# Optimization experiments

Measured on AMD Instinct MI355X. Metric: run time of the kernel, lower is better.

Reference implementation:

```python
import jax, jax.numpy as jnp
import numpy as np

DIM = 1024
HEADS = 16
SCALE = DIM ** (-0.5)  # NOTE: module scales by full dim, not head_dim


def setup_inputs() -> dict:
    key = jax.random.key(0)
    k1, k2, k3, k4 = jax.random.split(key, 4)
    x = jax.random.normal(k1, (4, 2048, DIM), dtype=jnp.float32)
    # torch Linear weights: y = x @ W.T
    w_qkv = jax.random.normal(k2, (3 * DIM, DIM), dtype=jnp.float32) * (DIM ** -0.5)
    w_out = jax.random.normal(k3, (DIM, DIM), dtype=jnp.float32) * (DIM ** -0.5)
    b_out = jax.random.normal(k4, (DIM,), dtype=jnp.float32) * 0.01
    return {"x": x, "w_qkv": w_qkv, "w_out": w_out, "b_out": b_out}


def reference(x, w_qkv, w_out, b_out):
    b, n, _ = x.shape
    h = HEADS
    d = DIM // h
    qkv = x @ w_qkv.T                                   # [b, n, 3*dim]
    qkv = qkv.reshape(b, n, 3, h, d)                    # split (qkv h d)
    qkv = jnp.transpose(qkv, (2, 0, 3, 1, 4))           # [3, b, h, n, d]
    q, k, v = qkv[0], qkv[1], qkv[2]
    dots = jnp.einsum('bhid,bhjd->bhij', q, k) * SCALE  # [b, h, n, n]
    attn = jax.nn.softmax(dots, axis=-1)
    out = jnp.einsum('bhij,bhjd->bhid', attn, v)        # [b, h, n, d]
    out = jnp.transpose(out, (0, 2, 1, 3)).reshape(b, n, h * d)
    return out @ w_out.T + b_out
```

## Files before the change

### kernel.cpp

```cpp
#include <hip/hip_runtime.h>

typedef short bf16x8 __attribute__((ext_vector_type(8)));
typedef _Float16 f16x8 __attribute__((ext_vector_type(8)));
typedef __fp16 fp16x2 __attribute__((ext_vector_type(2)));
typedef float f32x4 __attribute__((ext_vector_type(4)));
typedef float f32x16 __attribute__((ext_vector_type(16)));
typedef unsigned u32x2 __attribute__((ext_vector_type(2)));

static __device__ __forceinline__ unsigned short f2bf(float f) {
  union { float f; unsigned u; } v; v.f = f;
  unsigned r = v.u + 0x7fffu + ((v.u >> 16) & 1u);
  return (unsigned short)(r >> 16);
}

static __device__ __forceinline__ unsigned short f2h(float f) {
  union { _Float16 h; unsigned short u; } c; c.h = (_Float16)f; return c.u;
}

static __device__ __forceinline__ unsigned pkh(float lo, float hi) {
  union { fp16x2 h; unsigned u; } c;
  c.h = __builtin_amdgcn_cvt_pkrtz(lo, hi);
  return c.u;
}

static __device__ __forceinline__ void gll16(const unsigned short* g,
                                             unsigned short* l) {
  __builtin_amdgcn_global_load_lds(
      (const __attribute__((address_space(1))) unsigned int*)g,
      (__attribute__((address_space(3))) unsigned int*)l, 16, 0, 0);
}

__global__ void cvt3_kernel(const float* __restrict__ a,
                            const float* __restrict__ b,
                            const float* __restrict__ c,
                            unsigned short* __restrict__ dst) {
  int i = blockIdx.x * blockDim.x + threadIdx.x;
  const float* src; int off;
  if (i < 2097152) { src = a; off = 0; }
  else if (i < 2883584) { src = b; off = 2097152; }
  else { src = c; off = 2883584; }
  float4 f = ((const float4*)src)[i - off];
  ushort4 o;
  o.x = f2bf(f.x); o.y = f2bf(f.y); o.z = f2bf(f.z); o.w = f2bf(f.w);
  ((ushort4*)dst)[i] = o;
}

#define TM 128
#define TN 128
#define BK 64

template <int EPI>
__global__ __launch_bounds__(256, 2)
void gemm_bt(const unsigned short* __restrict__ X,
             const unsigned short* __restrict__ W,
             unsigned short* __restrict__ QKV, float* __restrict__ OUT,
             const float* __restrict__ bias, int M, int N, int K) {
  __shared__ __align__(16) unsigned short As[TM * BK];
  __shared__ __align__(16) unsigned short Bs[TN * BK];

  const int tid = threadIdx.x;
  const int lane = tid & 63;
  const int wave = tid >> 6;
  const int quad = lane >> 4;
  const int l16 = lane & 15;
  const int wm = wave >> 1, wn = wave & 1;
  const int rc = l16 & 7;

  const int m0 = blockIdx.y * TM;
  const int n0 = blockIdx.x * TN;

  const int sr = lane >> 3;
  const int gsc = ((lane & 7) ^ sr) * 8;

  f32x4 zero = {0.f, 0.f, 0.f, 0.f};
  f32x4 acc[4][4];
#pragma unroll
  for (int i = 0; i < 4; i++)
#pragma unroll
    for (int j = 0; j < 4; j++) acc[i][j] = zero;

  for (int k0 = 0; k0 < K; k0 += BK) {
    __syncthreads();
#pragma unroll
    for (int c = 0; c < 4; c++) {
      int row = wave * 32 + c * 8;
      gll16(&X[(size_t)(m0 + row + sr) * K + k0 + gsc], &As[row * BK]);
      gll16(&W[(size_t)(n0 + row + sr) * K + k0 + gsc], &Bs[row * BK]);
    }
    __syncthreads();
#pragma unroll
    for (int kk = 0; kk < 2; kk++) {
      bf16x8 af[4], bfr[4];
      const int csw = ((kk * 4 + quad) ^ rc) * 8;
#pragma unroll
      for (int t = 0; t < 4; t++) {
        af[t]  = *(const bf16x8*)&As[(wm * 64 + t * 16 + l16) * BK + csw];
        bfr[t] = *(const bf16x8*)&Bs[(wn * 64 + t * 16 + l16) * BK + csw];
      }
#pragma unroll
      for (int mt = 0; mt < 4; mt++)
#pragma unroll
        for (int nt = 0; nt < 4; nt++)
          acc[mt][nt] = __builtin_amdgcn_mfma_f32_16x16x32_bf16(
              af[mt], bfr[nt], acc[mt][nt], 0, 0, 0);
    }
  }

#pragma unroll
  for (int mt = 0; mt < 4; mt++) {
#pragma unroll
    for (int nt = 0; nt < 4; nt++) {
      if (EPI == 0) {
        int nbase = n0 + wn * 64 + nt * 16;
        int which = nbase >> 10;
        if (which == 2) {
          int rem = (nbase + l16) & 1023;
          int h = rem >> 6, dd = rem & 63;
          int growb = m0 + wm * 64 + mt * 16 + quad * 4;
          int b = growb >> 11, nn0 = growb & 2047;
          ushort4 o;
          o.x = f2h(acc[mt][nt][0]);
          o.y = f2h(acc[mt][nt][1]);
          o.z = f2h(acc[mt][nt][2]);
          o.w = f2h(acc[mt][nt][3]);
          *(ushort4*)&QKV[16777216u + (((size_t)(b * 16 + h) * 64 + dd) << 11) + nn0] = o;
        } else {
#pragma unroll
          for (int r = 0; r < 4; r++) {
            int grow = m0 + wm * 64 + mt * 16 + quad * 4 + r;
            int gcol = nbase + l16;
            int rem = gcol & 1023;
            int h = rem >> 6, dd = rem & 63;
            float v = acc[mt][nt][r];
            if (which == 0) v *= 0.04508422f;
            int b = grow >> 11, nn = grow & 2047;
            QKV[(size_t)which * 8388608 +
                ((size_t)(b * 16 + h) * 2048 + nn) * 64 + dd] = f2bf(v);
          }
        }
      } else {
#pragma unroll
        for (int r = 0; r < 4; r++) {
          int grow = m0 + wm * 64 + mt * 16 + quad * 4 + r;
          int gcol = n0 + wn * 64 + nt * 16 + l16;
          OUT[(size_t)grow * N + gcol] = acc[mt][nt][r] + bias[gcol];
        }
      }
    }
  }
}

#define SK 72

__global__ __launch_bounds__(512, 4)
void attn_kernel(const unsigned short* __restrict__ Qg,
                 const unsigned short* __restrict__ Kg,
                 const unsigned short* __restrict__ Vg,
                 unsigned short* __restrict__ AO) {
  __shared__ __align__(16) unsigned short K_s[2][64 * SK];
  __shared__ __align__(16) unsigned short V_s[2][64 * SK];

  const int tid = threadIdx.x;
  const int lane = tid & 63;
  const int wave = tid >> 6;
  const int l31 = lane & 31;
  const int hh = lane >> 5;

  const int id = blockIdx.x + 8 * blockIdx.y;
  const int xcd = id & 7;
  const int slot = id >> 3;
  const int bh = xcd * 8 + (slot & 7);
  const int qb = slot >> 3;

  const size_t base = (size_t)bh * 131072;
  const int q0 = qb * 256 + wave * 32;

  bf16x8 bq[4];
#pragma unroll
  for (int ks = 0; ks < 4; ks++)
    bq[ks] = *(const bf16x8*)&Qg[base + (size_t)(q0 + l31) * 64 + ks * 16 + hh * 8];

  f32x16 O[2];
#pragma unroll
  for (int dt = 0; dt < 2; dt++)
#pragma unroll
    for (int r = 0; r < 16; r++) O[dt][r] = 0.f;
  float lrow = 0.f;

  const int sr = lane >> 3, sc = (lane & 7) * 8;
  const unsigned short* Kp = Kg + base + (size_t)(wave * 8 + sr) * 64 + sc;
  const unsigned short* Vp = Vg + base + (size_t)(wave * 8 + sr) * 2048 + sc;
  const int woff = (wave * 8 + sr) * SK + sc;

  uint4 kr, vr;
  kr = *(const uint4*)Kp;
  vr = *(const uint4*)Vp;
  *(uint4*)&K_s[0][woff] = kr;
  *(uint4*)&V_s[0][woff] = vr;
  __syncthreads();

  for (int t = 0; t < 32; t++) {
    const unsigned short* Kc = K_s[t & 1];
    const unsigned short* Vc = V_s[t & 1];
    if (t < 31) {
      kr = *(const uint4*)(Kp + (size_t)(t + 1) * 4096);
      vr = *(const uint4*)(Vp + (size_t)(t + 1) * 64);
    }

    f32x16 S[2];
#pragma unroll
    for (int sub = 0; sub < 2; sub++) {
      f32x16 a;
#pragma unroll
      for (int r = 0; r < 16; r++) a[r] = 0.f;
#pragma unroll
      for (int ks = 0; ks < 4; ks++) {
        bf16x8 kf = *(const bf16x8*)&Kc[(sub * 32 + l31) * SK + ks * 16 + hh * 8];
        a = __builtin_amdgcn_mfma_f32_32x32x16_bf16(kf, bq[ks], a, 0, 0, 0);
      }
      S[sub] = a;
    }

    float rsum = 0.f;
#pragma unroll
    for (int sub = 0; sub < 2; sub++)
#pragma unroll
      for (int r = 0; r < 16; r++) {
        float p = __builtin_amdgcn_exp2f(S[sub][r]);
        S[sub][r] = p;
        rsum += p;
      }
    lrow += rsum;

#pragma unroll
    for (int win = 0; win < 4; win++) {
      const int sub = win >> 1, kk = win & 1;
      const int g0 = kk * 2, g1 = kk * 2 + 1;
      unsigned a00 = pkh(S[sub][4 * g0 + 0], S[sub][4 * g0 + 1]);
      unsigned a01 = pkh(S[sub][4 * g0 + 2], S[sub][4 * g0 + 3]);
      unsigned a10 = pkh(S[sub][4 * g1 + 0], S[sub][4 * g1 + 1]);
      unsigned a11 = pkh(S[sub][4 * g1 + 2], S[sub][4 * g1 + 3]);
      union { unsigned u[4]; f16x8 v; } fr;
#if __has_builtin(__builtin_amdgcn_permlane32_swap)
      u32x2 r0 = __builtin_amdgcn_permlane32_swap(a00, a10, false, false);
      u32x2 r1 = __builtin_amdgcn_permlane32_swap(a01, a11, false, false);
      fr.u[0] = r0.x; fr.u[1] = r1.x; fr.u[2] = r0.y; fr.u[3] = r1.y;
#else
      unsigned b00 = __shfl_xor((int)a00, 32);
      unsigned b01 = __shfl_xor((int)a01, 32);
      unsigned b10 = __shfl_xor((int)a10, 32);
      unsigned b11 = __shfl_xor((int)a11, 32);
      fr.u[0] = hh ? b10 : a00;
      fr.u[1] = hh ? b11 : a01;
      fr.u[2] = hh ? a10 : b00;
      fr.u[3] = hh ? a11 : b01;
#endif
      f16x8 pf = fr.v;
#pragma unroll
      for (int dt = 0; dt < 2; dt++) {
        f16x8 vf = *(const f16x8*)&Vc[(dt * 32 + l31) * SK + win * 16 + hh * 8];
        O[dt] = __builtin_amdgcn_mfma_f32_32x32x16_f16(vf, pf, O[dt], 0, 0, 0);
      }
    }

    if (t < 31) {
      const int nb = (t + 1) & 1;
      *(uint4*)&K_s[nb][woff] = kr;
      *(uint4*)&V_s[nb][woff] = vr;
    }
    __syncthreads();
  }

  const int b4 = bh >> 4, head = bh & 15;
  lrow += __shfl_xor(lrow, 32);
  float inv = 1.0f / lrow;
  int row = b4 * 2048 + q0 + l31;
#pragma unroll
  for (int dt = 0; dt < 2; dt++)
#pragma unroll
    for (int g = 0; g < 4; g++) {
      ushort4 o;
      o.x = f2bf(O[dt][4 * g + 0] * inv);
      o.y = f2bf(O[dt][4 * g + 1] * inv);
      o.z = f2bf(O[dt][4 * g + 2] * inv);
      o.w = f2bf(O[dt][4 * g + 3] * inv);
      *(ushort4*)&AO[(size_t)row * 1024 + head * 64 + dt * 32 + 8 * g + 4 * hh] = o;
    }
}

extern "C" void kernel_launch(void* const* d_in, const int* in_sizes, int n_in,
                              void* d_out, int out_size, void* d_ws,
                              size_t ws_size, hipStream_t stream) {
  const float* x     = (const float*)d_in[0];
  const float* w_qkv = (const float*)d_in[1];
  const float* w_out = (const float*)d_in[2];
  const float* b_out = (const float*)d_in[3];
  float* out = (float*)d_out;

  unsigned short* ws = (unsigned short*)d_ws;
  unsigned short* Xbf  = ws;
  unsigned short* Wqkv = ws + 8388608;
  unsigned short* Wout = ws + 11534336;
  unsigned short* QKV  = ws + 12582912;
  unsigned short* AO   = ws;

  cvt3_kernel<<<12288, 256, 0, stream>>>(x, w_qkv, w_out, Xbf);

  gemm_bt<0><<<dim3(3072 / TN, 8192 / TM), 256, 0, stream>>>(
      Xbf, Wqkv, QKV, nullptr, nullptr, 8192, 3072, 1024);

  attn_kernel<<<dim3(8, 64), 512, 0, stream>>>(
      QKV, QKV + 8388608, QKV + 16777216, AO);

  gemm_bt<1><<<dim3(1024 / TN, 8192 / TM), 256, 0, stream>>>(
      AO, Wout, nullptr, out, b_out, 8192, 1024, 1024);
}
```

Before: 251.2 us.

## Halve attention block size to 4 waves and add MFMA priority hints

The attention kernel now runs 256-thread blocks covering 128 queries each, in a 16x64 grid, and remaps block ids so the XCD grouping still works. Each thread stages two K/V rows per tile to fill the 64-row shared buffers. The MFMA sections are wrapped in s_setprio raises, and the first QK MFMA takes a zero constant instead of an explicitly zeroed accumulator. The intent is more, smaller blocks per CU for better scheduling and less barrier stall per block, at the cost of twice the K/V loads from global memory per query.

```diff
diff --git a/kernel.cpp b/kernel.cpp
--- a/kernel.cpp
+++ b/kernel.cpp
@@ -152,7 +152,7 @@
 
 #define SK 72
 
-__global__ __launch_bounds__(512, 4)
+__global__ __launch_bounds__(256, 4)
 void attn_kernel(const unsigned short* __restrict__ Qg,
                  const unsigned short* __restrict__ Kg,
                  const unsigned short* __restrict__ Vg,
@@ -166,60 +166,66 @@
   const int l31 = lane & 31;
   const int hh = lane >> 5;
 
-  const int id = blockIdx.x + 8 * blockIdx.y;
+  const int id = blockIdx.x + 16 * blockIdx.y;
   const int xcd = id & 7;
   const int slot = id >> 3;
   const int bh = xcd * 8 + (slot & 7);
   const int qb = slot >> 3;
 
   const size_t base = (size_t)bh * 131072;
-  const int q0 = qb * 256 + wave * 32;
+  const int q0 = qb * 128 + wave * 32;
 
   bf16x8 bq[4];
 #pragma unroll
   for (int ks = 0; ks < 4; ks++)
     bq[ks] = *(const bf16x8*)&Qg[base + (size_t)(q0 + l31) * 64 + ks * 16 + hh * 8];
 
+  f32x16 z16;
+#pragma unroll
+  for (int r = 0; r < 16; r++) z16[r] = 0.f;
+
   f32x16 O[2];
 #pragma unroll
-  for (int dt = 0; dt < 2; dt++)
-#pragma unroll
-    for (int r = 0; r < 16; r++) O[dt][r] = 0.f;
+  for (int dt = 0; dt < 2; dt++) O[dt] = z16;
   float lrow = 0.f;
 
   const int sr = lane >> 3, sc = (lane & 7) * 8;
-  const unsigned short* Kp = Kg + base + (size_t)(wave * 8 + sr) * 64 + sc;
-  const unsigned short* Vp = Vg + base + (size_t)(wave * 8 + sr) * 2048 + sc;
-  const int woff = (wave * 8 + sr) * SK + sc;
-
-  uint4 kr, vr;
-  kr = *(const uint4*)Kp;
-  vr = *(const uint4*)Vp;
-  *(uint4*)&K_s[0][woff] = kr;
-  *(uint4*)&V_s[0][woff] = vr;
+  const int r0 = wave * 8 + sr;
+  const unsigned short* Kp = Kg + base + (size_t)r0 * 64 + sc;
+  const unsigned short* Vp = Vg + base + (size_t)r0 * 2048 + sc;
+  const int woff = r0 * SK + sc;
+
+  uint4 kr0, kr1, vr0, vr1;
+  kr0 = *(const uint4*)Kp;           kr1 = *(const uint4*)(Kp + 2048);
+  vr0 = *(const uint4*)Vp;           vr1 = *(const uint4*)(Vp + 65536);
+  *(uint4*)&K_s[0][woff] = kr0;      *(uint4*)&K_s[0][woff + 32 * SK] = kr1;
+  *(uint4*)&V_s[0][woff] = vr0;      *(uint4*)&V_s[0][woff + 32 * SK] = vr1;
   __syncthreads();
 
   for (int t = 0; t < 32; t++) {
     const unsigned short* Kc = K_s[t & 1];
     const unsigned short* Vc = V_s[t & 1];
     if (t < 31) {
-      kr = *(const uint4*)(Kp + (size_t)(t + 1) * 4096);
-      vr = *(const uint4*)(Vp + (size_t)(t + 1) * 64);
+      const unsigned short* kp = Kp + (size_t)(t + 1) * 4096;
+      const unsigned short* vp = Vp + (size_t)(t + 1) * 64;
+      kr0 = *(const uint4*)kp;  kr1 = *(const uint4*)(kp + 2048);
+      vr0 = *(const uint4*)vp;  vr1 = *(const uint4*)(vp + 65536);
     }
 
     f32x16 S[2];
+    __builtin_amdgcn_s_setprio(1);
 #pragma unroll
     for (int sub = 0; sub < 2; sub++) {
-      f32x16 a;
-#pragma unroll
-      for (int r = 0; r < 16; r++) a[r] = 0.f;
-#pragma unroll
-      for (int ks = 0; ks < 4; ks++) {
+      bf16x8 kf0 = *(const bf16x8*)&Kc[(sub * 32 + l31) * SK + hh * 8];
+      f32x16 a = __builtin_amdgcn_mfma_f32_32x32x16_bf16(kf0, bq[0], z16, 0, 0, 0);
+#pragma unroll
+      for (int ks = 1; ks < 4; ks++) {
         bf16x8 kf = *(const bf16x8*)&Kc[(sub * 32 + l31) * SK + ks * 16 + hh * 8];
         a = __builtin_amdgcn_mfma_f32_32x32x16_bf16(kf, bq[ks], a, 0, 0, 0);
       }
       S[sub] = a;
     }
+    __builtin_amdgcn_s_setprio(0);
 
     float rsum = 0.f;
 #pragma unroll
@@ -232,6 +238,7 @@
       }
     lrow += rsum;
 
+    __builtin_amdgcn_s_setprio(1);
 #pragma unroll
     for (int win = 0; win < 4; win++) {
       const int sub = win >> 1, kk = win & 1;
@@ -262,11 +269,12 @@
         O[dt] = __builtin_amdgcn_mfma_f32_32x32x16_f16(vf, pf, O[dt], 0, 0, 0);
       }
     }
+    __builtin_amdgcn_s_setprio(0);
 
     if (t < 31) {
       const int nb = (t + 1) & 1;
-      *(uint4*)&K_s[nb][woff] = kr;
-      *(uint4*)&V_s[nb][woff] = vr;
+      *(uint4*)&K_s[nb][woff] = kr0;  *(uint4*)&K_s[nb][woff + 32 * SK] = kr1;
+      *(uint4*)&V_s[nb][woff] = vr0;  *(uint4*)&V_s[nb][woff + 32 * SK] = vr1;
     }
     __syncthreads();
   }
@@ -309,7 +317,7 @@
   gemm_bt<0><<<dim3(3072 / TN, 8192 / TM), 256, 0, stream>>>(
       Xbf, Wqkv, QKV, nullptr, nullptr, 8192, 3072, 1024);
 
-  attn_kernel<<<dim3(8, 64), 512, 0, stream>>>(
+  attn_kernel<<<dim3(16, 64), 256, 0, stream>>>(
       QKV, QKV + 8388608, QKV + 16777216, AO);
 
   gemm_bt<1><<<dim3(1024 / TN, 8192 / TM), 256, 0, stream>>>(
```

New measurement: 252.4 us. No clear change (+0.5%).

## Load K via async global-to-LDS with XOR swizzle, read V directly from global

Applied to the files above, without the earlier changes.

The attention kernel now stages only K in shared memory, using direct global-to-LDS loads (gll16) with an XOR swizzle in place of padded rows. V fragments are read straight from global memory into registers, one batch before the S MFMAs and one after the softmax. Blocks shrink from 512 to 256 threads with twice as many blocks, and LDS use drops. This removes the register round-trip and the V shared-memory staging, at the cost of uncoalesced-ish per-lane global V reads and more K re-reads across blocks.

```diff
diff --git a/kernel.cpp b/kernel.cpp
--- a/kernel.cpp
+++ b/kernel.cpp
@@ -150,15 +150,12 @@
   }
 }
 
-#define SK 72
-
-__global__ __launch_bounds__(512, 4)
+__global__ __launch_bounds__(256, 4)
 void attn_kernel(const unsigned short* __restrict__ Qg,
                  const unsigned short* __restrict__ Kg,
                  const unsigned short* __restrict__ Vg,
                  unsigned short* __restrict__ AO) {
-  __shared__ __align__(16) unsigned short K_s[2][64 * SK];
-  __shared__ __align__(16) unsigned short V_s[2][64 * SK];
+  __shared__ __align__(16) unsigned short K_s[2][64 * 64];
 
   const int tid = threadIdx.x;
   const int lane = tid & 63;
@@ -166,14 +163,14 @@
   const int l31 = lane & 31;
   const int hh = lane >> 5;
 
-  const int id = blockIdx.x + 8 * blockIdx.y;
+  const int id = blockIdx.x + 16 * blockIdx.y;
   const int xcd = id & 7;
   const int slot = id >> 3;
   const int bh = xcd * 8 + (slot & 7);
   const int qb = slot >> 3;
 
   const size_t base = (size_t)bh * 131072;
-  const int q0 = qb * 256 + wave * 32;
+  const int q0 = qb * 128 + wave * 32;
 
   bf16x8 bq[4];
 #pragma unroll
@@ -187,25 +184,33 @@
     for (int r = 0; r < 16; r++) O[dt][r] = 0.f;
   float lrow = 0.f;
 
-  const int sr = lane >> 3, sc = (lane & 7) * 8;
-  const unsigned short* Kp = Kg + base + (size_t)(wave * 8 + sr) * 64 + sc;
-  const unsigned short* Vp = Vg + base + (size_t)(wave * 8 + sr) * 2048 + sc;
-  const int woff = (wave * 8 + sr) * SK + sc;
-
-  uint4 kr, vr;
-  kr = *(const uint4*)Kp;
-  vr = *(const uint4*)Vp;
-  *(uint4*)&K_s[0][woff] = kr;
-  *(uint4*)&V_s[0][woff] = vr;
+  const int sr = lane >> 3;
+  const int gsc = ((lane & 7) ^ sr) * 8;
+  const int kxor = l31 & 7;
+
+#pragma unroll
+  for (int c = 0; c < 2; c++) {
+    int row = wave * 16 + c * 8;
+    gll16(&Kg[base + (size_t)(row + sr) * 64 + gsc], &K_s[0][row * 64]);
+  }
   __syncthreads();
 
   for (int t = 0; t < 32; t++) {
     const unsigned short* Kc = K_s[t & 1];
-    const unsigned short* Vc = V_s[t & 1];
     if (t < 31) {
-      kr = *(const uint4*)(Kp + (size_t)(t + 1) * 4096);
-      vr = *(const uint4*)(Vp + (size_t)(t + 1) * 64);
-    }
+#pragma unroll
+      for (int c = 0; c < 2; c++) {
+        int row = wave * 16 + c * 8;
+        gll16(&Kg[base + (size_t)((t + 1) * 64 + row + sr) * 64 + gsc],
+              &K_s[(t + 1) & 1][row * 64]);
+      }
+    }
+
+    f16x8 vf0[4];
+#pragma unroll
+    for (int win = 0; win < 4; win++)
+      vf0[win] = *(const f16x8*)&Vg[base + (size_t)l31 * 2048 +
+                                    t * 64 + win * 16 + hh * 8];
 
     f32x16 S[2];
 #pragma unroll
@@ -215,7 +220,8 @@
       for (int r = 0; r < 16; r++) a[r] = 0.f;
 #pragma unroll
       for (int ks = 0; ks < 4; ks++) {
-        bf16x8 kf = *(const bf16x8*)&Kc[(sub * 32 + l31) * SK + ks * 16 + hh * 8];
+        bf16x8 kf = *(const bf16x8*)&Kc[(sub * 32 + l31) * 64 +
+                                        (((ks * 2 + hh) ^ kxor) * 8)];
         a = __builtin_amdgcn_mfma_f32_32x32x16_bf16(kf, bq[ks], a, 0, 0, 0);
       }
       S[sub] = a;
@@ -231,6 +237,12 @@
         rsum += p;
       }
     lrow += rsum;
+
+    f16x8 vf1[4];
+#pragma unroll
+    for (int win = 0; win < 4; win++)
+      vf1[win] = *(const f16x8*)&Vg[base + (size_t)(32 + l31) * 2048 +
+                                    t * 64 + win * 16 + hh * 8];
 
 #pragma unroll
     for (int win = 0; win < 4; win++) {
@@ -256,18 +268,10 @@
       fr.u[3] = hh ? a11 : b01;
 #endif
       f16x8 pf = fr.v;
-#pragma unroll
-      for (int dt = 0; dt < 2; dt++) {
-        f16x8 vf = *(const f16x8*)&Vc[(dt * 32 + l31) * SK + win * 16 + hh * 8];
-        O[dt] = __builtin_amdgcn_mfma_f32_32x32x16_f16(vf, pf, O[dt], 0, 0, 0);
-      }
-    }
-
-    if (t < 31) {
-      const int nb = (t + 1) & 1;
-      *(uint4*)&K_s[nb][woff] = kr;
-      *(uint4*)&V_s[nb][woff] = vr;
-    }
+      O[0] = __builtin_amdgcn_mfma_f32_32x32x16_f16(vf0[win], pf, O[0], 0, 0, 0);
+      O[1] = __builtin_amdgcn_mfma_f32_32x32x16_f16(vf1[win], pf, O[1], 0, 0, 0);
+    }
+
     __syncthreads();
   }
 
@@ -309,7 +313,7 @@
   gemm_bt<0><<<dim3(3072 / TN, 8192 / TM), 256, 0, stream>>>(
       Xbf, Wqkv, QKV, nullptr, nullptr, 8192, 3072, 1024);
 
-  attn_kernel<<<dim3(8, 64), 512, 0, stream>>>(
+  attn_kernel<<<dim3(16, 64), 256, 0, stream>>>(
       QKV, QKV + 8388608, QKV + 16777216, AO);
 
   gemm_bt<1><<<dim3(1024 / TN, 8192 / TM), 256, 0, stream>>>(
```

New measurement: 318.0 us. +26.6%, slower.
